# Optimization experiments

Measured on AMD Instinct MI355X. Metric: run time of the kernel, lower is better.

Reference implementation:

```python
import jax, jax.numpy as jnp
import numpy as np

INPUT_SIZE = 512
HIDDEN_SIZE = 1024
BATCH = 16384


def setup_inputs() -> dict:
    key = jax.random.key(0)
    ks = jax.random.split(key, 11)
    s_x = 1.0 / np.sqrt(INPUT_SIZE)
    s_h = 1.0 / np.sqrt(HIDDEN_SIZE)
    inp = {
        "x": jax.random.normal(ks[0], (BATCH, INPUT_SIZE), dtype=jnp.float32),
        "hidden": jax.random.normal(ks[1], (BATCH, HIDDEN_SIZE), dtype=jnp.float32),
        # Linear weights stored as (in, out) for x @ W
        "Wxr": jax.random.uniform(ks[2], (INPUT_SIZE, HIDDEN_SIZE), jnp.float32, -s_x, s_x),
        "bxr": jax.random.uniform(ks[3], (HIDDEN_SIZE,), jnp.float32, -s_x, s_x),
        "Whr": jax.random.uniform(ks[4], (HIDDEN_SIZE, HIDDEN_SIZE), jnp.float32, -s_h, s_h),
        "Wxz": jax.random.uniform(ks[5], (INPUT_SIZE, HIDDEN_SIZE), jnp.float32, -s_x, s_x),
        "bxz": jax.random.uniform(ks[6], (HIDDEN_SIZE,), jnp.float32, -s_x, s_x),
        "Whz": jax.random.uniform(ks[7], (HIDDEN_SIZE, HIDDEN_SIZE), jnp.float32, -s_h, s_h),
        "Wxh": jax.random.uniform(ks[8], (INPUT_SIZE, HIDDEN_SIZE), jnp.float32, -s_x, s_x),
        "bxh": jax.random.uniform(ks[9], (HIDDEN_SIZE,), jnp.float32, -s_x, s_x),
        "Whh": jax.random.uniform(ks[10], (HIDDEN_SIZE, HIDDEN_SIZE), jnp.float32, -s_h, s_h),
    }
    return inp


def reference(x, hidden, Wxr, bxr, Whr, Wxz, bxz, Whz, Wxh, bxh, Whh):
    # GRU cell, single timestep.
    r = jax.nn.sigmoid(x @ Wxr + bxr + hidden @ Whr)          # reset gate (B,H)
    z = jax.nn.sigmoid(x @ Wxz + bxz + hidden @ Whz)          # update gate (B,H)
    h_cand = jnp.tanh(x @ Wxh + bxh + (r * hidden) @ Whh)     # candidate (B,H)
    return z * hidden + (1.0 - z) * h_cand
```

## Files before the change

kernel.cpp:

```cpp
#include <hip/hip_runtime.h>

typedef unsigned short u16;
typedef unsigned int u32;
typedef __bf16 bf16x8 __attribute__((ext_vector_type(8)));
typedef float f32x4 __attribute__((ext_vector_type(4)));

#define B_ROWS 16384
#define K1 1536

__device__ __forceinline__ u16 f2bf(float f) {
  u32 u = __float_as_uint(f);
  u = (u + 0x7fffu + ((u >> 16) & 1u)) >> 16;
  return (u16)u;
}
__device__ __forceinline__ float bf2f(u16 b) {
  return __uint_as_float(((u32)b) << 16);
}
__device__ __forceinline__ void gload_lds16(const void* g, void* l) {
  __builtin_amdgcn_global_load_lds((const __attribute__((address_space(1))) void*)g,
                                   (__attribute__((address_space(3))) void*)l,
                                   16, 0, 0);
}

__global__ void prep(const float* __restrict__ x, const float* __restrict__ h,
                     u16* __restrict__ xh,
                     const float* __restrict__ Wxr, const float* __restrict__ Whr,
                     const float* __restrict__ Wxz, const float* __restrict__ Whz,
                     const float* __restrict__ Wxh, const float* __restrict__ Whh,
                     u16* __restrict__ W1t, u16* __restrict__ W2t) {
  if (blockIdx.x < 24576) {
    const int iv = blockIdx.x * 256 + threadIdx.x;
    const int row = iv / 384;
    const int col = (iv - row * 384) * 4;
    const float* src = (col < 512) ? x + (size_t)row * 512 + col
                                   : h + (size_t)row * 1024 + (col - 512);
    float4 v = *(const float4*)src;
    u32 a = (u32)f2bf(v.x) | ((u32)f2bf(v.y) << 16);
    u32 b = (u32)f2bf(v.z) | ((u32)f2bf(v.w) << 16);
    *(uint2*)(xh + (size_t)row * 1536 + col) = make_uint2(a, b);
    return;
  }
  __shared__ float tile[32][33];
  const int idx2 = blockIdx.x - 24576;
  const int z = idx2 >> 10;
  const int rem = idx2 & 1023;
  const int by = rem >> 5, bx = rem & 31;
  const float* W;
  u16* T;
  int Ks, koff, roff;
  switch (z) {
    case 0:  W = Wxr; T = W1t; Ks = 512;  koff = 0;   roff = 0;    break;
    case 1:  W = Whr; T = W1t; Ks = 1024; koff = 512; roff = 0;    break;
    case 2:  W = Wxz; T = W1t; Ks = 512;  koff = 0;   roff = 1024; break;
    case 3:  W = Whz; T = W1t; Ks = 1024; koff = 512; roff = 1024; break;
    case 4:  W = Wxh; T = W2t; Ks = 512;  koff = 0;   roff = 0;    break;
    default: W = Whh; T = W2t; Ks = 1024; koff = 512; roff = 0;    break;
  }
  if (by * 32 >= Ks) return;
  const int tx = threadIdx.x & 31, ty = threadIdx.x >> 5;
#pragma unroll
  for (int r = 0; r < 32; r += 8)
    tile[ty + r][tx] = W[(size_t)(by * 32 + ty + r) * 1024 + bx * 32 + tx];
  __syncthreads();
#pragma unroll
  for (int r = 0; r < 32; r += 8)
    T[(size_t)(roff + bx * 32 + ty + r) * K1 + koff + by * 32 + tx] = f2bf(tile[tx][ty + r]);
}

__global__ __launch_bounds__(256, 2) void gru_gemm1(
    const u16* __restrict__ xh, const u16* __restrict__ W1t,
    const float* __restrict__ bxr, const float* __restrict__ bxz,
    u16* __restrict__ rhb, u16* __restrict__ zb) {
  __shared__ __align__(16) u16 As[128 * 32];
  __shared__ __align__(16) u16 Bs[128 * 32];
  const int orig = blockIdx.x;
  const int slot = orig >> 3;
  const int jt = slot & 15;
  const int mt = (orig & 7) + 8 * (slot >> 4);
  const int brow = mt * 128;
  const int bcol = jt * 128;

  const int tid = threadIdx.x;
  const int l = tid & 63;
  const int wid = tid >> 6;
  const int wrq = wid >> 1, wcq = wid & 1;
  const int lr = l & 15, kq = l >> 4;
  const int colK = (kq * 16) ^ (((lr >> 1) & 3) * 16);
  const int kswzE = ((tid & 3) ^ ((tid >> 3) & 3)) * 8;
  const int r = tid >> 2;
  char* AsB = (char*)As;
  char* BsB = (char*)Bs;
  const int ldsW = wid << 10;
  int aRow[4], bRow[4];
#pragma unroll
  for (int m = 0; m < 4; ++m) aRow[m] = (wrq * 64 + m * 16 + lr) * 64;
#pragma unroll
  for (int n = 0; n < 4; ++n) bRow[n] = (wcq * 64 + n * 16 + lr) * 64;

  u32 offA[2], offB[2];
#pragma unroll
  for (int q = 0; q < 2; ++q) {
    offA[q] = (u32)((brow + q * 64 + r) * K1 + kswzE) * 2u;
    offB[q] = (u32)((bcol + q * 64 + r) * K1 + kswzE) * 2u;
  }

  f32x4 acc[4][4] = {};
  for (int t = 0; t < 48; ++t) {
    gload_lds16((const char*)xh + offA[0], AsB + ldsW);
    gload_lds16((const char*)xh + offA[1], AsB + 4096 + ldsW);
    gload_lds16((const char*)W1t + offB[0], BsB + ldsW);
    gload_lds16((const char*)W1t + offB[1], BsB + 4096 + ldsW);
    asm volatile("s_waitcnt vmcnt(0)" ::: "memory");
    __builtin_amdgcn_s_barrier();
    asm volatile("" ::: "memory");
    bf16x8 a[4], b[4];
#pragma unroll
    for (int m = 0; m < 4; ++m) a[m] = *(const bf16x8*)(AsB + aRow[m] + colK);
#pragma unroll
    for (int n = 0; n < 4; ++n) b[n] = *(const bf16x8*)(BsB + bRow[n] + colK);
    asm volatile("s_waitcnt lgkmcnt(0)" ::: "memory");
    __builtin_amdgcn_sched_barrier(0);
    __builtin_amdgcn_s_setprio(1);
#pragma unroll
    for (int m = 0; m < 4; ++m)
#pragma unroll
      for (int n = 0; n < 4; ++n)
        acc[m][n] = __builtin_amdgcn_mfma_f32_16x16x32_bf16(a[m], b[n], acc[m][n], 0, 0, 0);
    __builtin_amdgcn_s_setprio(0);
    __builtin_amdgcn_s_barrier();
    asm volatile("" ::: "memory");
    offA[0] += 64; offA[1] += 64; offB[0] += 64; offB[1] += 64;
  }

  const int colb = (jt & 7) * 128 + wcq * 64 + (l & 15);
  const int rowb = brow + wrq * 64 + (l >> 4) * 4;
  if (jt < 8) {
#pragma unroll
    for (int n = 0; n < 4; ++n) {
      const int col = colb + n * 16;
      const float bias = bxr[col];
#pragma unroll
      for (int m = 0; m < 4; ++m)
#pragma unroll
        for (int j = 0; j < 4; ++j) {
          const int row = rowb + m * 16 + j;
          const float rg = 1.f / (1.f + __expf(-(acc[m][n][j] + bias)));
          const float hv = bf2f(xh[(size_t)row * K1 + 512 + col]);
          rhb[(size_t)row * 1024 + col] = f2bf(rg * hv);
        }
    }
  } else {
#pragma unroll
    for (int n = 0; n < 4; ++n) {
      const int col = colb + n * 16;
      const float bias = bxz[col];
#pragma unroll
      for (int m = 0; m < 4; ++m)
#pragma unroll
        for (int j = 0; j < 4; ++j) {
          const int row = rowb + m * 16 + j;
          const float zg = 1.f / (1.f + __expf(-(acc[m][n][j] + bias)));
          zb[(size_t)row * 1024 + col] = f2bf(zg);
        }
    }
  }
}

__global__ __launch_bounds__(512, 1) void gru_gemm2(
    const u16* __restrict__ xh, const u16* __restrict__ rhb,
    const u16* __restrict__ W2t, const float* __restrict__ bxh,
    const u16* __restrict__ zb, float* __restrict__ out) {
  __shared__ __align__(16) u16 As[2 * 256 * 64];
  __shared__ __align__(16) u16 Bs[2 * 128 * 64];
  const int orig = blockIdx.x;
  const int wg = (orig & 7) * 64 + (orig >> 3);
  const int mt = wg & 63;
  const int jt = wg >> 6;
  const int brow = mt * 256;
  const int jcol = jt * 128;

  const int tid = threadIdx.x;
  const int l = tid & 63;
  const int wid = tid >> 6;
  const int wrk = wid >> 1, wc = wid & 1;
  const int lr = l & 15, kq = l >> 4;
  const int swzB = (lr & 7) * 16;
  const int kswzE = ((tid & 7) ^ ((tid >> 3) & 7)) * 8;
  const int r = tid >> 3;
  char* AsB = (char*)As;
  char* BsB = (char*)Bs;
  const int ldsQ = wid << 10;
  const int colK0 = (kq * 16) ^ swzB;
  const int colK1 = (64 + kq * 16) ^ swzB;
  int aRow[4], bRow[4];
#pragma unroll
  for (int m = 0; m < 4; ++m) aRow[m] = (wrk * 64 + m * 16 + lr) * 128;
#pragma unroll
  for (int n = 0; n < 4; ++n) bRow[n] = (wc * 64 + n * 16 + lr) * 128;

  const u16* pA01 = xh;
  const u16* pA23 = xh;
  u32 offA[4], offB[2];
#pragma unroll
  for (int q = 0; q < 4; ++q) offA[q] = (u32)((brow + q * 64 + r) * K1 + kswzE) * 2u;
#pragma unroll
  for (int q = 0; q < 2; ++q) offB[q] = (u32)((jcol + q * 64 + r) * K1 + kswzE) * 2u;

#define G2_A01(q_, c_) gload_lds16((const char*)pA01 + offA[q_], \
    AsB + (c_) * 32768 + (q_) * 8192 + ldsQ)
#define G2_A23(q_, c_) gload_lds16((const char*)pA23 + offA[q_], \
    AsB + (c_) * 32768 + 16384 + ((q_) - 2) * 8192 + ldsQ)
#define G2_B(q_, c_)   gload_lds16((const char*)W2t + offB[q_], \
    BsB + (c_) * 16384 + (q_) * 8192 + ldsQ)

  G2_A01(0, 0); G2_A01(1, 0);
  G2_A23(2, 0); G2_A23(3, 0);
  G2_B(0, 0); G2_B(1, 0);
  offA[0] += 128; offA[1] += 128;
  G2_A01(0, 1); G2_A01(1, 1);
  offA[0] += 128; offA[1] += 128;
  offA[2] += 128; offA[3] += 128;
  offB[0] += 128; offB[1] += 128;
  asm volatile("s_waitcnt vmcnt(2)" ::: "memory");
  __builtin_amdgcn_s_barrier();
  asm volatile("" ::: "memory");

  f32x4 acc[4][4] = {};
  const int nt = 24;
  for (int t = 0; t < nt; ++t) {
    const int c = t & 1;
    const int cbA = c << 15;
    const int cbB = c << 14;
    bf16x8 a01[2][2], a23[2][2], b01[2][2], b23[2][2];
#pragma unroll
    for (int m = 0; m < 2; ++m) {
      a01[m][0] = *(const bf16x8*)(AsB + cbA + aRow[m] + colK0);
      a01[m][1] = *(const bf16x8*)(AsB + cbA + aRow[m] + colK1);
    }
#pragma unroll
    for (int n = 0; n < 2; ++n) {
      b01[n][0] = *(const bf16x8*)(BsB + cbB + bRow[n] + colK0);
      b01[n][1] = *(const bf16x8*)(BsB + cbB + bRow[n] + colK1);
    }
    if (t + 1 < nt) { G2_A23(2, c ^ 1); G2_A23(3, c ^ 1); }
    __builtin_amdgcn_s_barrier();
    asm volatile("s_waitcnt lgkmcnt(0)" ::: "memory");
    __builtin_amdgcn_sched_barrier(0);
    __builtin_amdgcn_s_setprio(1);
#pragma unroll
    for (int kk = 0; kk < 2; ++kk)
#pragma unroll
      for (int m = 0; m < 2; ++m)
#pragma unroll
        for (int n = 0; n < 2; ++n)
          acc[m][n] = __builtin_amdgcn_mfma_f32_16x16x32_bf16(a01[m][kk], b01[n][kk], acc[m][n], 0, 0, 0);
    __builtin_amdgcn_s_setprio(0);
    __builtin_amdgcn_s_barrier();
    asm volatile("" ::: "memory");
#pragma unroll
    for (int n = 0; n < 2; ++n) {
      b23[n][0] = *(const bf16x8*)(BsB + cbB + bRow[n + 2] + colK0);
      b23[n][1] = *(const bf16x8*)(BsB + cbB + bRow[n + 2] + colK1);
    }
    if (t + 1 < nt) { G2_B(0, c ^ 1); G2_B(1, c ^ 1); }
    __builtin_amdgcn_s_barrier();
    asm volatile("s_waitcnt lgkmcnt(0)" ::: "memory");
    __builtin_amdgcn_sched_barrier(0);
    __builtin_amdgcn_s_setprio(1);
#pragma unroll
    for (int kk = 0; kk < 2; ++kk)
#pragma unroll
      for (int m = 0; m < 2; ++m)
#pragma unroll
        for (int n = 0; n < 2; ++n)
          acc[m][n + 2] = __builtin_amdgcn_mfma_f32_16x16x32_bf16(a01[m][kk], b23[n][kk], acc[m][n + 2], 0, 0, 0);
    __builtin_amdgcn_s_setprio(0);
    __builtin_amdgcn_s_barrier();
    asm volatile("" ::: "memory");
#pragma unroll
    for (int m = 0; m < 2; ++m) {
      a23[m][0] = *(const bf16x8*)(AsB + cbA + aRow[m + 2] + colK0);
      a23[m][1] = *(const bf16x8*)(AsB + cbA + aRow[m + 2] + colK1);
    }
    __builtin_amdgcn_s_barrier();
    asm volatile("s_waitcnt lgkmcnt(0)" ::: "memory");
    __builtin_amdgcn_sched_barrier(0);
    __builtin_amdgcn_s_setprio(1);
#pragma unroll
    for (int kk = 0; kk < 2; ++kk)
#pragma unroll
      for (int m = 0; m < 2; ++m)
#pragma unroll
        for (int n = 0; n < 2; ++n)
          acc[m + 2][n + 2] = __builtin_amdgcn_mfma_f32_16x16x32_bf16(a23[m][kk], b23[n][kk], acc[m + 2][n + 2], 0, 0, 0);
    __builtin_amdgcn_s_setprio(0);
    __builtin_amdgcn_s_barrier();
    asm volatile("" ::: "memory");
    if (t + 2 < nt) { G2_A01(0, c); G2_A01(1, c); }
    __builtin_amdgcn_s_barrier();
    __builtin_amdgcn_s_setprio(1);
#pragma unroll
    for (int kk = 0; kk < 2; ++kk)
#pragma unroll
      for (int m = 0; m < 2; ++m)
#pragma unroll
        for (int n = 0; n < 2; ++n)
          acc[m + 2][n] = __builtin_amdgcn_mfma_f32_16x16x32_bf16(a23[m][kk], b01[n][kk], acc[m + 2][n], 0, 0, 0);
    __builtin_amdgcn_s_setprio(0);
    if (t + 2 < nt) { asm volatile("s_waitcnt vmcnt(2)" ::: "memory"); }
    else            { asm volatile("s_waitcnt vmcnt(0)" ::: "memory"); }
    __builtin_amdgcn_s_barrier();
    asm volatile("" ::: "memory");
    if (t == 5) {
      pA01 = rhb;
      offA[0] = (u32)((brow + 0 * 64 + r) * 1024 + kswzE) * 2u;
      offA[1] = (u32)((brow + 1 * 64 + r) * 1024 + kswzE) * 2u;
    } else { offA[0] += 128; offA[1] += 128; }
    if (t == 6) {
      pA23 = rhb;
      offA[2] = (u32)((brow + 2 * 64 + r) * 1024 + kswzE) * 2u;
      offA[3] = (u32)((brow + 3 * 64 + r) * 1024 + kswzE) * 2u;
    } else { offA[2] += 128; offA[3] += 128; }
    offB[0] += 128; offB[1] += 128;
  }
#undef G2_A01
#undef G2_A23
#undef G2_B

  const int colb = jcol + wc * 64 + (l & 15);
  const int rowb = brow + wrk * 64 + (l >> 4) * 4;
#pragma unroll
  for (int n = 0; n < 4; ++n) {
    const int col = colb + n * 16;
    const float bias = bxh[col];
#pragma unroll
    for (int m = 0; m < 4; ++m)
#pragma unroll
      for (int j = 0; j < 4; ++j) {
        const int row = rowb + m * 16 + j;
        const size_t idx = (size_t)row * 1024 + col;
        const float e = __expf(2.f * (acc[m][n][j] + bias));
        const float hc = 1.f - 2.f / (e + 1.f);
        const float z = bf2f(zb[idx]);
        const float h = bf2f(xh[(size_t)row * K1 + 512 + col]);
        out[idx] = z * h + (1.f - z) * hc;
      }
  }
}

extern "C" void kernel_launch(void* const* d_in, const int* in_sizes, int n_in,
                              void* d_out, int out_size, void* d_ws, size_t ws_size,
                              hipStream_t stream) {
  const float* x      = (const float*)d_in[0];
  const float* hidden = (const float*)d_in[1];
  const float* Wxr = (const float*)d_in[2];
  const float* bxr = (const float*)d_in[3];
  const float* Whr = (const float*)d_in[4];
  const float* Wxz = (const float*)d_in[5];
  const float* bxz = (const float*)d_in[6];
  const float* Whz = (const float*)d_in[7];
  const float* Wxh = (const float*)d_in[8];
  const float* bxh = (const float*)d_in[9];
  const float* Whh = (const float*)d_in[10];
  float* out = (float*)d_out;
  (void)in_sizes; (void)n_in; (void)out_size; (void)ws_size;

  char* p = (char*)d_ws;
  u16* xh  = (u16*)p; p += (size_t)B_ROWS * K1 * 2;
  u16* W1t = (u16*)p; p += (size_t)2048 * K1 * 2;
  u16* W2t = (u16*)p; p += (size_t)1024 * K1 * 2;
  u16* rhb = (u16*)p; p += (size_t)B_ROWS * 1024 * 2;
  u16* zb  = (u16*)p; p += (size_t)B_ROWS * 1024 * 2;

  prep<<<24576 + 6144, 256, 0, stream>>>(x, hidden, xh,
                                         Wxr, Whr, Wxz, Whz, Wxh, Whh, W1t, W2t);
  gru_gemm1<<<2048, 256, 0, stream>>>(xh, W1t, bxr, bxz, rhb, zb);
  gru_gemm2<<<512, 512, 0, stream>>>(xh, rhb, W2t, bxh, zb, out);
}
```

Measured before the change: 286.8 us.

## Reuse pipelined 256x128 double-buffered GEMM core for the gate GEMM

Pulls the double-buffered, software-pipelined 256x128 MFMA main loop out of gru_gemm2 into a shared device function and uses it for gru_gemm1 too. Previously gru_gemm1 used 128x128 tiles with one LDS buffer and a full vmcnt(0) wait each K step, so global loads never overlapped compute. gru_gemm1 now runs 1024 blocks of 512 threads with larger tiles and overlapped prefetch. In exchange it uses more LDS per block and runs one block per CU instead of two.

```diff
diff --git a/kernel.cpp b/kernel.cpp
--- a/kernel.cpp
+++ b/kernel.cpp
@@ -67,73 +67,183 @@
     T[(size_t)(roff + bx * 32 + ty + r) * K1 + koff + by * 32 + tx] = f2bf(tile[tx][ty + r]);
 }
 
-__global__ __launch_bounds__(256, 2) void gru_gemm1(
+struct CoreArgs {
+  const u16 *A, *A2, *B;
+  u32 sA, sA2, sB;
+  int tsw;
+};
+
+__device__ __forceinline__ void core256x128(const CoreArgs& C, int brow, int bcolB,
+                                            u16* AsU, u16* BsU, f32x4 acc[4][4]) {
+  const int tid = threadIdx.x;
+  const int l = tid & 63;
+  const int wid = tid >> 6;
+  const int lr = l & 15, kq = l >> 4;
+  const int wrk = wid >> 1, wc = wid & 1;
+  const int swzB = (lr & 7) * 16;
+  const int kswzE = ((tid & 7) ^ ((tid >> 3) & 7)) * 8;
+  const int r = tid >> 3;
+  char* AsB = (char*)AsU;
+  char* BsB = (char*)BsU;
+  const int ldsQ = wid << 10;
+  const int colK0 = (kq * 16) ^ swzB;
+  const int colK1 = (64 + kq * 16) ^ swzB;
+  int aRow[4], bRow[4];
+#pragma unroll
+  for (int m = 0; m < 4; ++m) aRow[m] = (wrk * 64 + m * 16 + lr) * 128;
+#pragma unroll
+  for (int n = 0; n < 4; ++n) bRow[n] = (wc * 64 + n * 16 + lr) * 128;
+
+  const u16* pA01 = C.A;
+  const u16* pA23 = C.A;
+  u32 offA[4], offB[2];
+#pragma unroll
+  for (int q = 0; q < 4; ++q) offA[q] = (u32)((brow + q * 64 + r) * C.sA + kswzE) * 2u;
+#pragma unroll
+  for (int q = 0; q < 2; ++q) offB[q] = (u32)((bcolB + q * 64 + r) * C.sB + kswzE) * 2u;
+
+#define C_A01(q_, c_) gload_lds16((const char*)pA01 + offA[q_], \
+    AsB + (c_) * 32768 + (q_) * 8192 + ldsQ)
+#define C_A23(q_, c_) gload_lds16((const char*)pA23 + offA[q_], \
+    AsB + (c_) * 32768 + 16384 + ((q_) - 2) * 8192 + ldsQ)
+#define C_B(q_, c_)   gload_lds16((const char*)C.B + offB[q_], \
+    BsB + (c_) * 16384 + (q_) * 8192 + ldsQ)
+
+  C_A01(0, 0); C_A01(1, 0);
+  C_A23(2, 0); C_A23(3, 0);
+  C_B(0, 0); C_B(1, 0);
+  offA[0] += 128; offA[1] += 128;
+  C_A01(0, 1); C_A01(1, 1);
+  offA[0] += 128; offA[1] += 128;
+  offA[2] += 128; offA[3] += 128;
+  offB[0] += 128; offB[1] += 128;
+  asm volatile("s_waitcnt vmcnt(2)" ::: "memory");
+  __builtin_amdgcn_s_barrier();
+  asm volatile("" ::: "memory");
+
+  const int nt = 24;
+  for (int t = 0; t < nt; ++t) {
+    const int c = t & 1;
+    const int cbA = c << 15;
+    const int cbB = c << 14;
+    bf16x8 a01[2][2], a23[2][2], b01[2][2], b23[2][2];
+#pragma unroll
+    for (int m = 0; m < 2; ++m) {
+      a01[m][0] = *(const bf16x8*)(AsB + cbA + aRow[m] + colK0);
+      a01[m][1] = *(const bf16x8*)(AsB + cbA + aRow[m] + colK1);
+    }
+#pragma unroll
+    for (int n = 0; n < 2; ++n) {
+      b01[n][0] = *(const bf16x8*)(BsB + cbB + bRow[n] + colK0);
+      b01[n][1] = *(const bf16x8*)(BsB + cbB + bRow[n] + colK1);
+    }
+    if (t + 1 < nt) { C_A23(2, c ^ 1); C_A23(3, c ^ 1); }
+    __builtin_amdgcn_s_barrier();
+    asm volatile("s_waitcnt lgkmcnt(0)" ::: "memory");
+    __builtin_amdgcn_sched_barrier(0);
+    __builtin_amdgcn_s_setprio(1);
+#pragma unroll
+    for (int kk = 0; kk < 2; ++kk)
+#pragma unroll
+      for (int m = 0; m < 2; ++m)
+#pragma unroll
+        for (int n = 0; n < 2; ++n)
+          acc[m][n] = __builtin_amdgcn_mfma_f32_16x16x32_bf16(a01[m][kk], b01[n][kk], acc[m][n], 0, 0, 0);
+    __builtin_amdgcn_s_setprio(0);
+    __builtin_amdgcn_s_barrier();
+    asm volatile("" ::: "memory");
+#pragma unroll
+    for (int n = 0; n < 2; ++n) {
+      b23[n][0] = *(const bf16x8*)(BsB + cbB + bRow[n + 2] + colK0);
+      b23[n][1] = *(const bf16x8*)(BsB + cbB + bRow[n + 2] + colK1);
+    }
+    if (t + 1 < nt) { C_B(0, c ^ 1); C_B(1, c ^ 1); }
+    __builtin_amdgcn_s_barrier();
+    asm volatile("s_waitcnt lgkmcnt(0)" ::: "memory");
+    __builtin_amdgcn_sched_barrier(0);
+    __builtin_amdgcn_s_setprio(1);
+#pragma unroll
+    for (int kk = 0; kk < 2; ++kk)
+#pragma unroll
+      for (int m = 0; m < 2; ++m)
+#pragma unroll
+        for (int n = 0; n < 2; ++n)
+          acc[m][n + 2] = __builtin_amdgcn_mfma_f32_16x16x32_bf16(a01[m][kk], b23[n][kk], acc[m][n + 2], 0, 0, 0);
+    __builtin_amdgcn_s_setprio(0);
+    __builtin_amdgcn_s_barrier();
+    asm volatile("" ::: "memory");
+#pragma unroll
+    for (int m = 0; m < 2; ++m) {
+      a23[m][0] = *(const bf16x8*)(AsB + cbA + aRow[m + 2] + colK0);
+      a23[m][1] = *(const bf16x8*)(AsB + cbA + aRow[m + 2] + colK1);
+    }
+    __builtin_amdgcn_s_barrier();
+    asm volatile("s_waitcnt lgkmcnt(0)" ::: "memory");
+    __builtin_amdgcn_sched_barrier(0);
+    __builtin_amdgcn_s_setprio(1);
+#pragma unroll
+    for (int kk = 0; kk < 2; ++kk)
+#pragma unroll
+      for (int m = 0; m < 2; ++m)
+#pragma unroll
+        for (int n = 0; n < 2; ++n)
+          acc[m + 2][n + 2] = __builtin_amdgcn_mfma_f32_16x16x32_bf16(a23[m][kk], b23[n][kk], acc[m + 2][n + 2], 0, 0, 0);
+    __builtin_amdgcn_s_setprio(0);
+    __builtin_amdgcn_s_barrier();
+    asm volatile("" ::: "memory");
+    if (t + 2 < nt) { C_A01(0, c); C_A01(1, c); }
+    __builtin_amdgcn_s_barrier();
+    __builtin_amdgcn_s_setprio(1);
+#pragma unroll
+    for (int kk = 0; kk < 2; ++kk)
+#pragma unroll
+      for (int m = 0; m < 2; ++m)
+#pragma unroll
+        for (int n = 0; n < 2; ++n)
+          acc[m + 2][n] = __builtin_amdgcn_mfma_f32_16x16x32_bf16(a23[m][kk], b01[n][kk], acc[m + 2][n], 0, 0, 0);
+    __builtin_amdgcn_s_setprio(0);
+    if (t + 2 < nt) { asm volatile("s_waitcnt vmcnt(2)" ::: "memory"); }
+    else            { asm volatile("s_waitcnt vmcnt(0)" ::: "memory"); }
+    __builtin_amdgcn_s_barrier();
+    asm volatile("" ::: "memory");
+    if (t == C.tsw - 3) {
+      pA01 = C.A2;
+      offA[0] = (u32)((brow + 0 * 64 + r) * C.sA2 + kswzE) * 2u;
+      offA[1] = (u32)((brow + 1 * 64 + r) * C.sA2 + kswzE) * 2u;
+    } else { offA[0] += 128; offA[1] += 128; }
+    if (t == C.tsw - 2) {
+      pA23 = C.A2;
+      offA[2] = (u32)((brow + 2 * 64 + r) * C.sA2 + kswzE) * 2u;
+      offA[3] = (u32)((brow + 3 * 64 + r) * C.sA2 + kswzE) * 2u;
+    } else { offA[2] += 128; offA[3] += 128; }
+    offB[0] += 128; offB[1] += 128;
+  }
+#undef C_A01
+#undef C_A23
+#undef C_B
+}
+
+__global__ __launch_bounds__(512, 1) void gru_gemm1(
     const u16* __restrict__ xh, const u16* __restrict__ W1t,
     const float* __restrict__ bxr, const float* __restrict__ bxz,
     u16* __restrict__ rhb, u16* __restrict__ zb) {
-  __shared__ __align__(16) u16 As[128 * 32];
-  __shared__ __align__(16) u16 Bs[128 * 32];
+  __shared__ __align__(16) u16 As[2 * 256 * 64];
+  __shared__ __align__(16) u16 Bs[2 * 128 * 64];
   const int orig = blockIdx.x;
   const int slot = orig >> 3;
   const int jt = slot & 15;
   const int mt = (orig & 7) + 8 * (slot >> 4);
-  const int brow = mt * 128;
-  const int bcol = jt * 128;
-
-  const int tid = threadIdx.x;
-  const int l = tid & 63;
-  const int wid = tid >> 6;
-  const int wrq = wid >> 1, wcq = wid & 1;
-  const int lr = l & 15, kq = l >> 4;
-  const int colK = (kq * 16) ^ (((lr >> 1) & 3) * 16);
-  const int kswzE = ((tid & 3) ^ ((tid >> 3) & 3)) * 8;
-  const int r = tid >> 2;
-  char* AsB = (char*)As;
-  char* BsB = (char*)Bs;
-  const int ldsW = wid << 10;
-  int aRow[4], bRow[4];
-#pragma unroll
-  for (int m = 0; m < 4; ++m) aRow[m] = (wrq * 64 + m * 16 + lr) * 64;
-#pragma unroll
-  for (int n = 0; n < 4; ++n) bRow[n] = (wcq * 64 + n * 16 + lr) * 64;
-
-  u32 offA[2], offB[2];
-#pragma unroll
-  for (int q = 0; q < 2; ++q) {
-    offA[q] = (u32)((brow + q * 64 + r) * K1 + kswzE) * 2u;
-    offB[q] = (u32)((bcol + q * 64 + r) * K1 + kswzE) * 2u;
-  }
-
+  const int brow = mt * 256;
+
+  CoreArgs C { xh, xh, W1t, K1, K1, K1, -100 };
   f32x4 acc[4][4] = {};
-  for (int t = 0; t < 48; ++t) {
-    gload_lds16((const char*)xh + offA[0], AsB + ldsW);
-    gload_lds16((const char*)xh + offA[1], AsB + 4096 + ldsW);
-    gload_lds16((const char*)W1t + offB[0], BsB + ldsW);
-    gload_lds16((const char*)W1t + offB[1], BsB + 4096 + ldsW);
-    asm volatile("s_waitcnt vmcnt(0)" ::: "memory");
-    __builtin_amdgcn_s_barrier();
-    asm volatile("" ::: "memory");
-    bf16x8 a[4], b[4];
-#pragma unroll
-    for (int m = 0; m < 4; ++m) a[m] = *(const bf16x8*)(AsB + aRow[m] + colK);
-#pragma unroll
-    for (int n = 0; n < 4; ++n) b[n] = *(const bf16x8*)(BsB + bRow[n] + colK);
-    asm volatile("s_waitcnt lgkmcnt(0)" ::: "memory");
-    __builtin_amdgcn_sched_barrier(0);
-    __builtin_amdgcn_s_setprio(1);
-#pragma unroll
-    for (int m = 0; m < 4; ++m)
-#pragma unroll
-      for (int n = 0; n < 4; ++n)
-        acc[m][n] = __builtin_amdgcn_mfma_f32_16x16x32_bf16(a[m], b[n], acc[m][n], 0, 0, 0);
-    __builtin_amdgcn_s_setprio(0);
-    __builtin_amdgcn_s_barrier();
-    asm volatile("" ::: "memory");
-    offA[0] += 64; offA[1] += 64; offB[0] += 64; offB[1] += 64;
-  }
-
-  const int colb = (jt & 7) * 128 + wcq * 64 + (l & 15);
-  const int rowb = brow + wrq * 64 + (l >> 4) * 4;
+  core256x128(C, brow, jt * 128, As, Bs, acc);
+
+  const int l = threadIdx.x & 63;
+  const int wid = threadIdx.x >> 6;
+  const int wrk = wid >> 1, wc = wid & 1;
+  const int colb = (jt & 7) * 128 + wc * 64 + (l & 15);
+  const int rowb = brow + wrk * 64 + (l >> 4) * 4;
   if (jt < 8) {
 #pragma unroll
     for (int n = 0; n < 4; ++n) {
@@ -179,154 +289,13 @@
   const int brow = mt * 256;
   const int jcol = jt * 128;
 
-  const int tid = threadIdx.x;
-  const int l = tid & 63;
-  const int wid = tid >> 6;
+  CoreArgs C { xh, rhb, W2t, K1, 1024, K1, 8 };
+  f32x4 acc[4][4] = {};
+  core256x128(C, brow, jcol, As, Bs, acc);
+
+  const int l = threadIdx.x & 63;
+  const int wid = threadIdx.x >> 6;
   const int wrk = wid >> 1, wc = wid & 1;
-  const int lr = l & 15, kq = l >> 4;
-  const int swzB = (lr & 7) * 16;
-  const int kswzE = ((tid & 7) ^ ((tid >> 3) & 7)) * 8;
-  const int r = tid >> 3;
-  char* AsB = (char*)As;
-  char* BsB = (char*)Bs;
-  const int ldsQ = wid << 10;
-  const int colK0 = (kq * 16) ^ swzB;
-  const int colK1 = (64 + kq * 16) ^ swzB;
-  int aRow[4], bRow[4];
-#pragma unroll
-  for (int m = 0; m < 4; ++m) aRow[m] = (wrk * 64 + m * 16 + lr) * 128;
-#pragma unroll
-  for (int n = 0; n < 4; ++n) bRow[n] = (wc * 64 + n * 16 + lr) * 128;
-
-  const u16* pA01 = xh;
-  const u16* pA23 = xh;
-  u32 offA[4], offB[2];
-#pragma unroll
-  for (int q = 0; q < 4; ++q) offA[q] = (u32)((brow + q * 64 + r) * K1 + kswzE) * 2u;
-#pragma unroll
-  for (int q = 0; q < 2; ++q) offB[q] = (u32)((jcol + q * 64 + r) * K1 + kswzE) * 2u;
-
-#define G2_A01(q_, c_) gload_lds16((const char*)pA01 + offA[q_], \
-    AsB + (c_) * 32768 + (q_) * 8192 + ldsQ)
-#define G2_A23(q_, c_) gload_lds16((const char*)pA23 + offA[q_], \
-    AsB + (c_) * 32768 + 16384 + ((q_) - 2) * 8192 + ldsQ)
-#define G2_B(q_, c_)   gload_lds16((const char*)W2t + offB[q_], \
-    BsB + (c_) * 16384 + (q_) * 8192 + ldsQ)
-
-  G2_A01(0, 0); G2_A01(1, 0);
-  G2_A23(2, 0); G2_A23(3, 0);
-  G2_B(0, 0); G2_B(1, 0);
-  offA[0] += 128; offA[1] += 128;
-  G2_A01(0, 1); G2_A01(1, 1);
-  offA[0] += 128; offA[1] += 128;
-  offA[2] += 128; offA[3] += 128;
-  offB[0] += 128; offB[1] += 128;
-  asm volatile("s_waitcnt vmcnt(2)" ::: "memory");
-  __builtin_amdgcn_s_barrier();
-  asm volatile("" ::: "memory");
-
-  f32x4 acc[4][4] = {};
-  const int nt = 24;
-  for (int t = 0; t < nt; ++t) {
-    const int c = t & 1;
-    const int cbA = c << 15;
-    const int cbB = c << 14;
-    bf16x8 a01[2][2], a23[2][2], b01[2][2], b23[2][2];
-#pragma unroll
-    for (int m = 0; m < 2; ++m) {
-      a01[m][0] = *(const bf16x8*)(AsB + cbA + aRow[m] + colK0);
-      a01[m][1] = *(const bf16x8*)(AsB + cbA + aRow[m] + colK1);
-    }
-#pragma unroll
-    for (int n = 0; n < 2; ++n) {
-      b01[n][0] = *(const bf16x8*)(BsB + cbB + bRow[n] + colK0);
-      b01[n][1] = *(const bf16x8*)(BsB + cbB + bRow[n] + colK1);
-    }
-    if (t + 1 < nt) { G2_A23(2, c ^ 1); G2_A23(3, c ^ 1); }
-    __builtin_amdgcn_s_barrier();
-    asm volatile("s_waitcnt lgkmcnt(0)" ::: "memory");
-    __builtin_amdgcn_sched_barrier(0);
-    __builtin_amdgcn_s_setprio(1);
-#pragma unroll
-    for (int kk = 0; kk < 2; ++kk)
-#pragma unroll
-      for (int m = 0; m < 2; ++m)
-#pragma unroll
-        for (int n = 0; n < 2; ++n)
-          acc[m][n] = __builtin_amdgcn_mfma_f32_16x16x32_bf16(a01[m][kk], b01[n][kk], acc[m][n], 0, 0, 0);
-    __builtin_amdgcn_s_setprio(0);
-    __builtin_amdgcn_s_barrier();
-    asm volatile("" ::: "memory");
-#pragma unroll
-    for (int n = 0; n < 2; ++n) {
-      b23[n][0] = *(const bf16x8*)(BsB + cbB + bRow[n + 2] + colK0);
-      b23[n][1] = *(const bf16x8*)(BsB + cbB + bRow[n + 2] + colK1);
-    }
-    if (t + 1 < nt) { G2_B(0, c ^ 1); G2_B(1, c ^ 1); }
-    __builtin_amdgcn_s_barrier();
-    asm volatile("s_waitcnt lgkmcnt(0)" ::: "memory");
-    __builtin_amdgcn_sched_barrier(0);
-    __builtin_amdgcn_s_setprio(1);
-#pragma unroll
-    for (int kk = 0; kk < 2; ++kk)
-#pragma unroll
-      for (int m = 0; m < 2; ++m)
-#pragma unroll
-        for (int n = 0; n < 2; ++n)
-          acc[m][n + 2] = __builtin_amdgcn_mfma_f32_16x16x32_bf16(a01[m][kk], b23[n][kk], acc[m][n + 2], 0, 0, 0);
-    __builtin_amdgcn_s_setprio(0);
-    __builtin_amdgcn_s_barrier();
-    asm volatile("" ::: "memory");
-#pragma unroll
-    for (int m = 0; m < 2; ++m) {
-      a23[m][0] = *(const bf16x8*)(AsB + cbA + aRow[m + 2] + colK0);
-      a23[m][1] = *(const bf16x8*)(AsB + cbA + aRow[m + 2] + colK1);
-    }
-    __builtin_amdgcn_s_barrier();
-    asm volatile("s_waitcnt lgkmcnt(0)" ::: "memory");
-    __builtin_amdgcn_sched_barrier(0);
-    __builtin_amdgcn_s_setprio(1);
-#pragma unroll
-    for (int kk = 0; kk < 2; ++kk)
-#pragma unroll
-      for (int m = 0; m < 2; ++m)
-#pragma unroll
-        for (int n = 0; n < 2; ++n)
-          acc[m + 2][n + 2] = __builtin_amdgcn_mfma_f32_16x16x32_bf16(a23[m][kk], b23[n][kk], acc[m + 2][n + 2], 0, 0, 0);
-    __builtin_amdgcn_s_setprio(0);
-    __builtin_amdgcn_s_barrier();
-    asm volatile("" ::: "memory");
-    if (t + 2 < nt) { G2_A01(0, c); G2_A01(1, c); }
-    __builtin_amdgcn_s_barrier();
-    __builtin_amdgcn_s_setprio(1);
-#pragma unroll
-    for (int kk = 0; kk < 2; ++kk)
-#pragma unroll
-      for (int m = 0; m < 2; ++m)
-#pragma unroll
-        for (int n = 0; n < 2; ++n)
-          acc[m + 2][n] = __builtin_amdgcn_mfma_f32_16x16x32_bf16(a23[m][kk], b01[n][kk], acc[m + 2][n], 0, 0, 0);
-    __builtin_amdgcn_s_setprio(0);
-    if (t + 2 < nt) { asm volatile("s_waitcnt vmcnt(2)" ::: "memory"); }
-    else            { asm volatile("s_waitcnt vmcnt(0)" ::: "memory"); }
-    __builtin_amdgcn_s_barrier();
-    asm volatile("" ::: "memory");
-    if (t == 5) {
-      pA01 = rhb;
-      offA[0] = (u32)((brow + 0 * 64 + r) * 1024 + kswzE) * 2u;
-      offA[1] = (u32)((brow + 1 * 64 + r) * 1024 + kswzE) * 2u;
-    } else { offA[0] += 128; offA[1] += 128; }
-    if (t == 6) {
-      pA23 = rhb;
-      offA[2] = (u32)((brow + 2 * 64 + r) * 1024 + kswzE) * 2u;
-      offA[3] = (u32)((brow + 3 * 64 + r) * 1024 + kswzE) * 2u;
-    } else { offA[2] += 128; offA[3] += 128; }
-    offB[0] += 128; offB[1] += 128;
-  }
-#undef G2_A01
-#undef G2_A23
-#undef G2_B
-
   const int colb = jcol + wc * 64 + (l & 15);
   const int rowb = brow + wrk * 64 + (l >> 4) * 4;
 #pragma unroll
@@ -374,6 +343,6 @@
 
   prep<<<24576 + 6144, 256, 0, stream>>>(x, hidden, xh,
                                          Wxr, Whr, Wxz, Whz, Wxh, Whh, W1t, W2t);
-  gru_gemm1<<<2048, 256, 0, stream>>>(xh, W1t, bxr, bxz, rhb, zb);
+  gru_gemm1<<<1024, 512, 0, stream>>>(xh, W1t, bxr, bxz, rhb, zb);
   gru_gemm2<<<512, 512, 0, stream>>>(xh, rhb, W2t, bxh, zb, out);
 }
```

Result: faster. 277.5 us (-3.2%).
